# Optimization experiments

Measured on AMD Instinct MI355X. Metric: run time of the kernel, lower is better.

The kernel has to match this reference:

```python
import jax, jax.numpy as jnp
import numpy as np

B, S, H = 32, 2048, 1024


def sparsemax(z, axis):
    # Martins & Astudillo (2016) sparsemax projection onto the simplex.
    n = z.shape[axis]
    z_sorted = -jnp.sort(-z, axis=axis)  # descending sort
    z_cum = jnp.cumsum(z_sorted, axis=axis)
    k = jnp.arange(1, n + 1, dtype=z.dtype).reshape(
        [n if i == (axis % z.ndim) else 1 for i in range(z.ndim)])
    support = (1.0 + k * z_sorted) > z_cum
    k_z = jnp.sum(support, axis=axis, keepdims=True)  # support size per row
    tau = (jnp.take_along_axis(z_cum, k_z.astype(jnp.int32) - 1, axis=axis) - 1.0) / k_z.astype(z.dtype)
    return jnp.maximum(z - tau, 0.0)


def setup_inputs() -> dict:
    key = jax.random.key(0)
    ks = jax.random.split(key, 8)
    s = 1.0 / np.sqrt(H)
    return {
        "encoder_output": jax.random.normal(ks[0], (B, S, H), jnp.float32),
        "decoder_hidden": jax.random.normal(ks[1], (B, H), jnp.float32),
        "Wa_w": jax.random.uniform(ks[2], (H, H), jnp.float32, -s, s),
        "Wa_b": jax.random.uniform(ks[3], (H,), jnp.float32, -s, s),
        "Ua_w": jax.random.uniform(ks[4], (H, H), jnp.float32, -s, s),
        "Ua_b": jax.random.uniform(ks[5], (H,), jnp.float32, -s, s),
        "Va_w": jax.random.uniform(ks[6], (1, H), jnp.float32, -s, s),
        "Va_b": jax.random.uniform(ks[7], (1,), jnp.float32, -s, s),
    }


def reference(encoder_output, decoder_hidden, Wa_w, Wa_b, Ua_w, Ua_b, Va_w, Va_b):
    # query: [B, 1, H]
    query = (decoder_hidden @ Wa_w.T + Wa_b)[:, None, :]
    # keys: [B, S, H]
    keys = jnp.einsum('bsh,oh->bso', encoder_output, Ua_w) + Ua_b
    # energy: [B, S]
    energy = jnp.einsum('bsh,h->bs', jnp.tanh(keys + query), Va_w[0]) + Va_b[0]
    attention_weights = sparsemax(energy, axis=1)  # [B, S]
    # context: [B, 1, H]
    context = jnp.einsum('bs,bsh->bh', attention_weights, encoder_output)[:, None, :]
    return (context, attention_weights)
```

## Files before the change

### kernel.cpp

```cpp
#include <hip/hip_runtime.h>
#include <stdint.h>
#include <stddef.h>

#define BB 32
#define SS 2048
#define HH 1024
#define MTOT (BB*SS)
#define NC 16

typedef _Float16 h8 __attribute__((ext_vector_type(8)));
typedef float f32x4 __attribute__((ext_vector_type(4)));

__device__ __forceinline__ void gload_lds16(const void* g, void* l) {
  __builtin_amdgcn_global_load_lds(
      (const __attribute__((address_space(1))) void*)g,
      (__attribute__((address_space(3))) void*)l,
      16, 0, 0);
}

__device__ __forceinline__ float fast_tanh(float x) {
  x = fminf(15.f, fmaxf(-15.f, x));
  float t = __expf(2.f * x);
  return (t - 1.f) * __builtin_amdgcn_rcpf(t + 1.f);
}

__global__ __launch_bounds__(256) void cvt_h(const float* __restrict__ src,
                                             _Float16* __restrict__ dst) {
  int t = blockIdx.x * 256 + threadIdx.x;
  const float4* s4 = (const float4*)src + (size_t)t * 2;
  float4 f0 = s4[0], f1 = s4[1];
  h8 v;
  v[0]=(_Float16)f0.x; v[1]=(_Float16)f0.y; v[2]=(_Float16)f0.z; v[3]=(_Float16)f0.w;
  v[4]=(_Float16)f1.x; v[5]=(_Float16)f1.y; v[6]=(_Float16)f1.z; v[7]=(_Float16)f1.w;
  *(h8*)(dst + (size_t)t * 8) = v;
}

__global__ __launch_bounds__(256) void cvt_h_big(const float* __restrict__ src,
                                                 _Float16* __restrict__ dst) {
#pragma unroll
  for (int i = 0; i < 8; ++i) {
    size_t t = ((size_t)(blockIdx.x + 4096 * i)) * 256 + threadIdx.x;
    const float4* s4 = (const float4*)src + t * 2;
    float4 f0 = s4[0], f1 = s4[1];
    h8 v;
    v[0]=(_Float16)f0.x; v[1]=(_Float16)f0.y; v[2]=(_Float16)f0.z; v[3]=(_Float16)f0.w;
    v[4]=(_Float16)f1.x; v[5]=(_Float16)f1.y; v[6]=(_Float16)f1.z; v[7]=(_Float16)f1.w;
    *(h8*)(dst + t * 8) = v;
  }
}

__global__ __launch_bounds__(256) void query_k(const float* __restrict__ dh,
                                               const float* __restrict__ Wa,
                                               const float* __restrict__ Wa_b,
                                               const float* __restrict__ Ua_b,
                                               float* __restrict__ qv) {
  int gw = (blockIdx.x * 256 + threadIdx.x) >> 6;
  int lane = threadIdx.x & 63;
  int o = gw >> 5;
  int b = gw & 31;
  const float4* x4 = (const float4*)(dh + (size_t)b * HH);
  const float4* w4 = (const float4*)(Wa + (size_t)o * HH);
  float s = 0.f;
#pragma unroll
  for (int j = 0; j < 4; ++j) {
    float4 a = x4[lane + 64 * j];
    float4 c = w4[lane + 64 * j];
    s += a.x * c.x + a.y * c.y + a.z * c.z + a.w * c.w;
  }
#pragma unroll
  for (int d = 32; d >= 1; d >>= 1) s += __shfl_xor(s, d, 64);
  if (lane == 0) qv[b * HH + o] = s + Wa_b[o] + Ua_b[o];
}

__global__ __launch_bounds__(256) void energy_gemm_h(const _Float16* __restrict__ Ahp,
                                                     const _Float16* __restrict__ Bh,
                                                     const float* __restrict__ qv,
                                                     const float* __restrict__ Va,
                                                     float* __restrict__ energy) {
  __shared__ __align__(16) _Float16 As[2][128 * 64];
  __shared__ __align__(16) _Float16 Bs[2][128 * 64];

  const int tid  = threadIdx.x;
  const int lane = tid & 63;
  const int w    = tid >> 6;
  const int wrow = (w & 1) * 64;
  const int wcol = (w >> 1) * 64;
  const int lr   = lane & 15;
  const int lq   = lane >> 4;

  const int x     = blockIdx.x;
  const int xcd   = x & 7;
  const int i6    = x >> 3;
  const int strip = xcd * 64 + (i6 >> 3);
  const int nblk  = i6 & 7;
  const int m0    = strip * 128;
  const int n0    = nblk * 128;

  f32x4 acc[4][4];
#pragma unroll
  for (int i = 0; i < 4; ++i)
#pragma unroll
    for (int j = 0; j < 4; ++j) acc[i][j] = (f32x4){0.f, 0.f, 0.f, 0.f};

#define STAGE(buf, kt_) do {                                                   \
    const int k0_ = (kt_) * 64;                                                \
    _Pragma("unroll")                                                          \
    for (int i_ = 0; i_ < 4; ++i_) {                                           \
      int g_ = tid + 256 * i_;                                                 \
      int r_ = g_ >> 3;                                                        \
      int c_ = (g_ & 7) ^ (r_ & 7);                                            \
      gload_lds16(Bh + (size_t)(n0 + r_) * HH + k0_ + c_ * 8,                  \
                  &Bs[buf][g_ * 8]);                                           \
      gload_lds16(Ahp + (size_t)(m0 + r_) * HH + k0_ + c_ * 8,                 \
                  &As[buf][g_ * 8]);                                           \
    }                                                                          \
  } while (0)

  STAGE(0, 0);
  __syncthreads();
  int cur = 0;

  for (int kt = 0; kt < 16; ++kt) {
    if (kt + 1 < 16) STAGE(cur ^ 1, kt + 1);
#pragma unroll
    for (int kk = 0; kk < 2; ++kk) {
      h8 af[4], bf[4];
#pragma unroll
      for (int i = 0; i < 4; ++i) {
        int ra = wrow + i * 16 + lr;
        int ca = kk * 4 + lq;
        af[i] = *(const h8*)&As[cur][(ra * 8 + (ca ^ (ra & 7))) * 8];
        int rb = wcol + i * 16 + lr;
        bf[i] = *(const h8*)&Bs[cur][(rb * 8 + (ca ^ (rb & 7))) * 8];
      }
#pragma unroll
      for (int i = 0; i < 4; ++i)
#pragma unroll
        for (int j = 0; j < 4; ++j)
          acc[i][j] = __builtin_amdgcn_mfma_f32_16x16x32_f16(af[i], bf[j], acc[i][j], 0, 0, 0);
    }
    __syncthreads();
    cur ^= 1;
  }
#undef STAGE

  const int bq = m0 >> 11;
  float qvv[4], vaw[4];
#pragma unroll
  for (int j = 0; j < 4; ++j) {
    int n = n0 + wcol + j * 16 + lr;
    qvv[j] = qv[bq * HH + n];
    vaw[j] = Va[n];
  }
#pragma unroll
  for (int i = 0; i < 4; ++i) {
    float p[4] = {0.f, 0.f, 0.f, 0.f};
#pragma unroll
    for (int j = 0; j < 4; ++j)
#pragma unroll
      for (int r = 0; r < 4; ++r)
        p[r] += fast_tanh(acc[i][j][r] + qvv[j]) * vaw[j];
#pragma unroll
    for (int r = 0; r < 4; ++r) {
      float v = p[r];
      v += __shfl_xor(v, 1, 64);
      v += __shfl_xor(v, 2, 64);
      v += __shfl_xor(v, 4, 64);
      v += __shfl_xor(v, 8, 64);
      if (lr == 0) {
        int m = m0 + wrow + i * 16 + lq * 4 + r;
        atomicAdd(&energy[m], v);
      }
    }
  }
}

__global__ __launch_bounds__(256) void energy_gemm_f32(const float* __restrict__ Ag,
                                                       const _Float16* __restrict__ Bh,
                                                       const float* __restrict__ qv,
                                                       const float* __restrict__ Va,
                                                       float* __restrict__ energy) {
  __shared__ __align__(16) _Float16 As[128 * 64];
  __shared__ __align__(16) _Float16 Bs[128 * 64];
  const int tid  = threadIdx.x;
  const int lane = tid & 63;
  const int w    = tid >> 6;
  const int wrow = (w & 1) * 64;
  const int wcol = (w >> 1) * 64;
  const int lr   = lane & 15;
  const int lq   = lane >> 4;
  const int x     = blockIdx.x;
  const int xcd   = x & 7;
  const int i6    = x >> 3;
  const int strip = xcd * 64 + (i6 >> 3);
  const int nblk  = i6 & 7;
  const int m0    = strip * 128;
  const int n0    = nblk * 128;
  f32x4 acc[4][4];
#pragma unroll
  for (int i = 0; i < 4; ++i)
#pragma unroll
    for (int j = 0; j < 4; ++j) acc[i][j] = (f32x4){0.f, 0.f, 0.f, 0.f};
  for (int kt = 0; kt < 16; ++kt) {
    const int k0 = kt * 64;
#pragma unroll
    for (int i = 0; i < 4; ++i) {
      int g = tid + 256 * i;
      int r = g >> 3;
      int c = (g & 7) ^ (r & 7);
      gload_lds16(Bh + (size_t)(n0 + r) * HH + k0 + c * 8, &Bs[g * 8]);
    }
    float4 fa[8];
#pragma unroll
    for (int i = 0; i < 4; ++i) {
      int g = tid + 256 * i;
      int r = g >> 3;
      int c = (g & 7) ^ (r & 7);
      const float* src = Ag + (size_t)(m0 + r) * HH + k0 + c * 8;
      fa[2 * i]     = *(const float4*)src;
      fa[2 * i + 1] = *(const float4*)(src + 4);
    }
#pragma unroll
    for (int i = 0; i < 4; ++i) {
      int g = tid + 256 * i;
      h8 v;
      v[0]=(_Float16)fa[2*i].x;   v[1]=(_Float16)fa[2*i].y;
      v[2]=(_Float16)fa[2*i].z;   v[3]=(_Float16)fa[2*i].w;
      v[4]=(_Float16)fa[2*i+1].x; v[5]=(_Float16)fa[2*i+1].y;
      v[6]=(_Float16)fa[2*i+1].z; v[7]=(_Float16)fa[2*i+1].w;
      *(h8*)&As[g * 8] = v;
    }
    __syncthreads();
#pragma unroll
    for (int kk = 0; kk < 2; ++kk) {
      h8 af[4], bf[4];
#pragma unroll
      for (int i = 0; i < 4; ++i) {
        int ra = wrow + i * 16 + lr;
        int ca = kk * 4 + lq;
        af[i] = *(const h8*)&As[(ra * 8 + (ca ^ (ra & 7))) * 8];
        int rb = wcol + i * 16 + lr;
        bf[i] = *(const h8*)&Bs[(rb * 8 + (ca ^ (rb & 7))) * 8];
      }
#pragma unroll
      for (int i = 0; i < 4; ++i)
#pragma unroll
        for (int j = 0; j < 4; ++j)
          acc[i][j] = __builtin_amdgcn_mfma_f32_16x16x32_f16(af[i], bf[j], acc[i][j], 0, 0, 0);
    }
    __syncthreads();
  }
  const int bq = m0 >> 11;
  float qvv[4], vaw[4];
#pragma unroll
  for (int j = 0; j < 4; ++j) {
    int n = n0 + wcol + j * 16 + lr;
    qvv[j] = qv[bq * HH + n];
    vaw[j] = Va[n];
  }
#pragma unroll
  for (int i = 0; i < 4; ++i) {
    float p[4] = {0.f, 0.f, 0.f, 0.f};
#pragma unroll
    for (int j = 0; j < 4; ++j)
#pragma unroll
      for (int r = 0; r < 4; ++r)
        p[r] += fast_tanh(acc[i][j][r] + qvv[j]) * vaw[j];
#pragma unroll
    for (int r = 0; r < 4; ++r) {
      float v = p[r];
      v += __shfl_xor(v, 1, 64);
      v += __shfl_xor(v, 2, 64);
      v += __shfl_xor(v, 4, 64);
      v += __shfl_xor(v, 8, 64);
      if (lr == 0) {
        int m = m0 + wrow + i * 16 + lq * 4 + r;
        atomicAdd(&energy[m], v);
      }
    }
  }
}

__global__ __launch_bounds__(256) void sparse_k(const float* __restrict__ energy,
                                                const float* __restrict__ Va_b,
                                                float* __restrict__ attn,
                                                int* __restrict__ scnt,
                                                int* __restrict__ ssidx,
                                                float* __restrict__ saval) {
  const int b = blockIdx.x;
  const int tid = threadIdx.x;
  const int lane = tid & 63;
  const int w = tid >> 6;
  __shared__ int cnt;
  if (tid == 0) cnt = 0;

  const float* z = energy + (size_t)b * SS;
  const float vb = Va_b[0];
  float zv[32];
#pragma unroll
  for (int k = 0; k < 32; ++k) zv[k] = z[lane + 64 * k] + vb;

  float mx = zv[0];
#pragma unroll
  for (int k = 1; k < 32; ++k) mx = fmaxf(mx, zv[k]);
#pragma unroll
  for (int d = 32; d >= 1; d >>= 1) mx = fmaxf(mx, __shfl_xor(mx, d, 64));

  float lo = mx - 1.f, hi = mx;
  for (int it = 0; it < 40; ++it) {
    float tau = 0.5f * (lo + hi);
    float ss = 0.f;
#pragma unroll
    for (int k = 0; k < 32; ++k) ss += fmaxf(zv[k] - tau, 0.f);
#pragma unroll
    for (int d = 32; d >= 1; d >>= 1) ss += __shfl_xor(ss, d, 64);
    if (ss >= 1.f) lo = tau; else hi = tau;
  }
  const float tau = 0.5f * (lo + hi);

  __syncthreads();
  int* si = ssidx + b * SS;
  float* av = saval + b * SS;
#pragma unroll
  for (int kk = 0; kk < 8; ++kk) {
    int k = w * 8 + kk;
    int s = lane + 64 * k;
    float a = fmaxf(zv[k] - tau, 0.f);
    attn[(size_t)b * SS + s] = a;
    if (a > 0.f) {
      int p = atomicAdd(&cnt, 1);
      si[p] = s;
      av[p] = a;
    }
  }
  __syncthreads();
  if (tid == 0) scnt[b] = cnt;
}

__global__ __launch_bounds__(256) void ctx_k(const float* __restrict__ enc,
                                             const int* __restrict__ scnt,
                                             const int* __restrict__ ssidx,
                                             const float* __restrict__ saval,
                                             float* __restrict__ ctx) {
  const int b = blockIdx.x >> 4;
  const int c = blockIdx.x & (NC - 1);
  const int tid = threadIdx.x;
  const int n = scnt[b];
  if (c >= n) return;

  const float* eb = enc + (size_t)b * SS * HH;
  const int* si = ssidx + b * SS;
  const float* av = saval + b * SS;

  float c0 = 0.f, c1 = 0.f, c2 = 0.f, c3 = 0.f;
  for (int p = c; p < n; p += NC) {
    float a = av[p];
    const float* row = eb + (size_t)si[p] * HH;
    c0 += a * row[tid];
    c1 += a * row[tid + 256];
    c2 += a * row[tid + 512];
    c3 += a * row[tid + 768];
  }
  atomicAdd(&ctx[(size_t)b * HH + tid],       c0);
  atomicAdd(&ctx[(size_t)b * HH + tid + 256], c1);
  atomicAdd(&ctx[(size_t)b * HH + tid + 512], c2);
  atomicAdd(&ctx[(size_t)b * HH + tid + 768], c3);
}

extern "C" void kernel_launch(void* const* d_in, const int* in_sizes, int n_in,
                              void* d_out, int out_size, void* d_ws, size_t ws_size,
                              hipStream_t stream) {
  const float* enc  = (const float*)d_in[0];
  const float* dh   = (const float*)d_in[1];
  const float* Wa_w = (const float*)d_in[2];
  const float* Wa_b = (const float*)d_in[3];
  const float* Ua_w = (const float*)d_in[4];
  const float* Ua_b = (const float*)d_in[5];
  const float* Va_w = (const float*)d_in[6];
  const float* Va_b = (const float*)d_in[7];

  float* out_ctx  = (float*)d_out;
  float* out_attn = (float*)d_out + BB * HH;

  char* ws = (char*)d_ws;
  _Float16* Ua_h = (_Float16*)ws;
  float* qv      = (float*)(ws + 2 * 1024 * 1024);
  float* energy  = (float*)(ws + 2 * 1024 * 1024 + 128 * 1024);
  int*   scnt    = (int*)  (ws + 2 * 1024 * 1024 + 512 * 1024);
  int*   ssidx   = (int*)  (ws + 2 * 1024 * 1024 + 516 * 1024);
  float* saval   = (float*)(ws + 2 * 1024 * 1024 + 772 * 1024);
  _Float16* enc_h = (_Float16*)(ws + 4 * 1024 * 1024);

  const size_t need_h = 4ull * 1024 * 1024 + (size_t)MTOT * HH * sizeof(_Float16);
  const bool use_ah = (ws_size >= need_h);

  if (use_ah) {
    cvt_h_big<<<4096, 256, 0, stream>>>(enc, enc_h);
  }
  cvt_h<<<512, 256, 0, stream>>>(Ua_w, Ua_h);
  query_k<<<8192, 256, 0, stream>>>(dh, Wa_w, Wa_b, Ua_b, qv);
  hipMemsetAsync(energy, 0, MTOT * sizeof(float), stream);
  hipMemsetAsync(out_ctx, 0, BB * HH * sizeof(float), stream);
  if (use_ah) {
    energy_gemm_h<<<4096, 256, 0, stream>>>(enc_h, Ua_h, qv, Va_w, energy);
  } else {
    energy_gemm_f32<<<4096, 256, 0, stream>>>(enc, Ua_h, qv, Va_w, energy);
  }
  sparse_k<<<BB, 256, 0, stream>>>(energy, Va_b, out_attn, scnt, ssidx, saval);
  ctx_k<<<BB * NC, 256, 0, stream>>>(enc, scnt, ssidx, saval, out_ctx);
}
```

Measured before the change: 674.7 us.

## Single-buffer energy GEMM with smaller K tile, simple conversion kernel

The fp16 energy GEMM goes from a double-buffered 64-wide K tile to a single-buffered 32-wide K tile with its own swizzle and incrementing pointers. This cuts LDS use so more workgroups can run per CU, at the cost of no load/compute overlap inside a block and twice as many barriers. The big encoder conversion kernel is replaced by the generic cvt_h launched with one element group per thread, and it now runs right before the GEMM.

Result: faster. 617.5 us (-8.5%).

```diff
diff --git a/kernel.cpp b/kernel.cpp
--- a/kernel.cpp
+++ b/kernel.cpp
@@ -33,20 +33,6 @@
   v[0]=(_Float16)f0.x; v[1]=(_Float16)f0.y; v[2]=(_Float16)f0.z; v[3]=(_Float16)f0.w;
   v[4]=(_Float16)f1.x; v[5]=(_Float16)f1.y; v[6]=(_Float16)f1.z; v[7]=(_Float16)f1.w;
   *(h8*)(dst + (size_t)t * 8) = v;
-}
-
-__global__ __launch_bounds__(256) void cvt_h_big(const float* __restrict__ src,
-                                                 _Float16* __restrict__ dst) {
-#pragma unroll
-  for (int i = 0; i < 8; ++i) {
-    size_t t = ((size_t)(blockIdx.x + 4096 * i)) * 256 + threadIdx.x;
-    const float4* s4 = (const float4*)src + t * 2;
-    float4 f0 = s4[0], f1 = s4[1];
-    h8 v;
-    v[0]=(_Float16)f0.x; v[1]=(_Float16)f0.y; v[2]=(_Float16)f0.z; v[3]=(_Float16)f0.w;
-    v[4]=(_Float16)f1.x; v[5]=(_Float16)f1.y; v[6]=(_Float16)f1.z; v[7]=(_Float16)f1.w;
-    *(h8*)(dst + t * 8) = v;
-  }
 }
 
 __global__ __launch_bounds__(256) void query_k(const float* __restrict__ dh,
@@ -77,8 +63,8 @@
                                                      const float* __restrict__ qv,
                                                      const float* __restrict__ Va,
                                                      float* __restrict__ energy) {
-  __shared__ __align__(16) _Float16 As[2][128 * 64];
-  __shared__ __align__(16) _Float16 Bs[2][128 * 64];
+  __shared__ __align__(16) _Float16 As[128 * 32];
+  __shared__ __align__(16) _Float16 Bs[128 * 32];
 
   const int tid  = threadIdx.x;
   const int lane = tid & 63;
@@ -102,47 +88,38 @@
 #pragma unroll
     for (int j = 0; j < 4; ++j) acc[i][j] = (f32x4){0.f, 0.f, 0.f, 0.f};
 
-#define STAGE(buf, kt_) do {                                                   \
-    const int k0_ = (kt_) * 64;                                                \
-    _Pragma("unroll")                                                          \
-    for (int i_ = 0; i_ < 4; ++i_) {                                           \
-      int g_ = tid + 256 * i_;                                                 \
-      int r_ = g_ >> 3;                                                        \
-      int c_ = (g_ & 7) ^ (r_ & 7);                                            \
-      gload_lds16(Bh + (size_t)(n0 + r_) * HH + k0_ + c_ * 8,                  \
-                  &Bs[buf][g_ * 8]);                                           \
-      gload_lds16(Ahp + (size_t)(m0 + r_) * HH + k0_ + c_ * 8,                 \
-                  &As[buf][g_ * 8]);                                           \
-    }                                                                          \
-  } while (0)
-
-  STAGE(0, 0);
-  __syncthreads();
-  int cur = 0;
-
-  for (int kt = 0; kt < 16; ++kt) {
-    if (kt + 1 < 16) STAGE(cur ^ 1, kt + 1);
-#pragma unroll
-    for (int kk = 0; kk < 2; ++kk) {
-      h8 af[4], bf[4];
-#pragma unroll
-      for (int i = 0; i < 4; ++i) {
-        int ra = wrow + i * 16 + lr;
-        int ca = kk * 4 + lq;
-        af[i] = *(const h8*)&As[cur][(ra * 8 + (ca ^ (ra & 7))) * 8];
-        int rb = wcol + i * 16 + lr;
-        bf[i] = *(const h8*)&Bs[cur][(rb * 8 + (ca ^ (rb & 7))) * 8];
-      }
-#pragma unroll
-      for (int i = 0; i < 4; ++i)
-#pragma unroll
-        for (int j = 0; j < 4; ++j)
-          acc[i][j] = __builtin_amdgcn_mfma_f32_16x16x32_f16(af[i], bf[j], acc[i][j], 0, 0, 0);
-    }
+  const int g0 = tid;
+  const int g1 = tid + 256;
+  const int r0 = g0 >> 2, c0 = (g0 & 3) ^ ((r0 >> 1) & 3);
+  const int r1 = g1 >> 2, c1 = (g1 & 3) ^ ((r1 >> 1) & 3);
+  const _Float16* ap0 = Ahp + (size_t)(m0 + r0) * HH + c0 * 8;
+  const _Float16* ap1 = Ahp + (size_t)(m0 + r1) * HH + c1 * 8;
+  const _Float16* bp0 = Bh  + (size_t)(n0 + r0) * HH + c0 * 8;
+  const _Float16* bp1 = Bh  + (size_t)(n0 + r1) * HH + c1 * 8;
+
+  for (int kt = 0; kt < 32; ++kt) {
+    gload_lds16(ap0, &As[g0 * 8]);
+    gload_lds16(ap1, &As[g1 * 8]);
+    gload_lds16(bp0, &Bs[g0 * 8]);
+    gload_lds16(bp1, &Bs[g1 * 8]);
     __syncthreads();
-    cur ^= 1;
-  }
-#undef STAGE
+
+    h8 af[4], bf[4];
+#pragma unroll
+    for (int i = 0; i < 4; ++i) {
+      int ra = wrow + i * 16 + lr;
+      af[i] = *(const h8*)&As[(ra * 4 + (lq ^ ((ra >> 1) & 3))) * 8];
+      int rb = wcol + i * 16 + lr;
+      bf[i] = *(const h8*)&Bs[(rb * 4 + (lq ^ ((rb >> 1) & 3))) * 8];
+    }
+#pragma unroll
+    for (int i = 0; i < 4; ++i)
+#pragma unroll
+      for (int j = 0; j < 4; ++j)
+        acc[i][j] = __builtin_amdgcn_mfma_f32_16x16x32_f16(af[i], bf[j], acc[i][j], 0, 0, 0);
+    __syncthreads();
+    ap0 += 32; ap1 += 32; bp0 += 32; bp1 += 32;
+  }
 
   const int bq = m0 >> 11;
   float qvv[4], vaw[4];
@@ -394,14 +371,12 @@
   const size_t need_h = 4ull * 1024 * 1024 + (size_t)MTOT * HH * sizeof(_Float16);
   const bool use_ah = (ws_size >= need_h);
 
-  if (use_ah) {
-    cvt_h_big<<<4096, 256, 0, stream>>>(enc, enc_h);
-  }
   cvt_h<<<512, 256, 0, stream>>>(Ua_w, Ua_h);
   query_k<<<8192, 256, 0, stream>>>(dh, Wa_w, Wa_b, Ua_b, qv);
   hipMemsetAsync(energy, 0, MTOT * sizeof(float), stream);
   hipMemsetAsync(out_ctx, 0, BB * HH * sizeof(float), stream);
   if (use_ah) {
+    cvt_h<<<32768, 256, 0, stream>>>(enc, enc_h);
     energy_gemm_h<<<4096, 256, 0, stream>>>(enc_h, Ua_h, qv, Va_w, energy);
   } else {
     energy_gemm_f32<<<4096, 256, 0, stream>>>(enc, Ua_h, qv, Va_w, energy);
```
